# Performance work log

Hardware: AMD Instinct MI355X
Metric: run time of the kernel (lower is better)

Reference implementation:

```python
import jax, jax.numpy as jnp
import numpy as np

SELF_DIM = 36
ENT_DIM = 28
HID = 256


def setup_inputs() -> dict:
    key = jax.random.key(0)
    ks = jax.random.split(key, 12)
    B, agent_num, n_noisy = 32768, 20, 20
    obs_dim = SELF_DIM + ENT_DIM * (2 * agent_num - 1 + n_noisy)
    s = 0.02
    return {
        "x": jax.random.normal(ks[0], (B, obs_dim), dtype=jnp.float32),
        "Watt": jax.random.normal(ks[1], (ENT_DIM + SELF_DIM, 1), jnp.float32) * s,
        "batt": jnp.zeros((1,), jnp.float32),
        "We": jax.random.normal(ks[2], (ENT_DIM + SELF_DIM, HID), jnp.float32) * s,
        "be": jnp.zeros((HID,), jnp.float32),
        "Wse": jax.random.normal(ks[3], (2 * SELF_DIM, HID), jnp.float32) * s,
        "bse": jnp.zeros((HID,), jnp.float32),
        "Wg": jax.random.normal(ks[4], (3 * HID, 3), jnp.float32) * s,
        "bg": jnp.zeros((3,), jnp.float32),
        "Wo": jax.random.normal(ks[5], (2 * HID, HID), jnp.float32) * s,
        "bo": jnp.zeros((HID,), jnp.float32),
        "agent_num": agent_num,
    }


def reference(x, Watt, batt, We, be, Wse, bse, Wg, bg, Wo, bo, agent_num):
    B = x.shape[0]
    self_info = x[:, :SELF_DIM]  # [B,36]
    opp_end = SELF_DIM + ENT_DIM * agent_num
    par_end = opp_end + ENT_DIM * (agent_num - 1)
    opps = x[:, SELF_DIM:opp_end].reshape(B, agent_num, ENT_DIM)
    pars = x[:, opp_end:par_end].reshape(B, agent_num - 1, ENT_DIM)
    noisy = x[:, par_end:].reshape(B, -1, ENT_DIM)

    def pool(ent):
        # additive-attention pooling over one entity group
        n = ent.shape[1]
        os_ = jnp.concatenate(
            [jnp.broadcast_to(self_info[:, None, :], (B, n, SELF_DIM)), ent], axis=2
        )  # [B,n,64]
        att = jax.nn.softmax(os_ @ Watt + batt, axis=1)  # [B,n,1]
        es = os_ @ We + be  # [B,n,H]
        return jnp.sum(att * es, axis=1)  # [B,H]

    opp_e, par_e, noi_e = pool(opps), pool(pars), pool(noisy)
    group_e = jnp.stack([opp_e, par_e, noi_e], axis=1)  # [B,3,H]
    gw = jax.nn.softmax(
        jnp.concatenate([opp_e, par_e, noi_e], axis=1) @ Wg + bg, axis=1
    )  # [B,3]
    other = jnp.einsum("bg,bgh->bh", gw, group_e)  # [B,H]
    self_e = jnp.concatenate([self_info, self_info], axis=1) @ Wse + bse  # [B,H]
    obs_embedding = jnp.concatenate([other, self_e], axis=1)  # [B,2H]
    return obs_embedding @ Wo + bo
```

## Files before the change

kernel.cpp:

```cpp
#include <hip/hip_runtime.h>
#include <hip/hip_bf16.h>

#define SELF_D 36
#define ENT_D  28
#define HID    256
#define OBS    1688
#define NWAVES 8192

#define WS_A     0
#define WS_B     9216
#define WS_C     16384
#define WS_MSEL  16640
#define WS_MENT  16748
#define WS_CG    17000
#define WS_WATT  17008
#define WS_AT    17040
#define WS_BT    26256
#define WS_TOTAL 33424

__global__ __launch_bounds__(256)
void setup_kernel(const float* __restrict__ Watt, const float* __restrict__ We,
                  const float* __restrict__ be,  const float* __restrict__ Wse,
                  const float* __restrict__ bse, const float* __restrict__ Wg,
                  const float* __restrict__ bg,  const float* __restrict__ Wo,
                  const float* __restrict__ bo,  float* __restrict__ ws) {
  const int blk = blockIdx.x;
  const int c = threadIdx.x;
  if (blk < 36) {
    int k = blk;
    float acc = 0.f;
    for (int r = 0; r < 256; ++r) acc += We[k*256 + r] * Wo[r*256 + c];
    for (int r = 0; r < 256; ++r) acc += (Wse[k*256 + r] + Wse[(36+k)*256 + r]) * Wo[(256+r)*256 + c];
    ws[WS_A + k*256 + c] = acc;
    ws[WS_AT + c*36 + k] = acc;
  } else if (blk < 64) {
    int k = blk - 36;
    float acc = 0.f;
    for (int r = 0; r < 256; ++r) acc += We[(36+k)*256 + r] * Wo[r*256 + c];
    ws[WS_B + k*256 + c] = acc;
    ws[WS_BT + c*28 + k] = acc;
  } else if (blk == 64) {
    float acc = bo[c];
    for (int r = 0; r < 256; ++r) acc += be[r] * Wo[r*256 + c];
    for (int r = 0; r < 256; ++r) acc += bse[r] * Wo[(256+r)*256 + c];
    ws[WS_C + c] = acc;
  } else {
    for (int t = c; t < 391; t += 256) {
      if (t < 108) {
        int k = t / 3, j = t - 3*k;
        float acc = 0.f;
        for (int r = 0; r < 256; ++r) {
          float wg = Wg[r*3 + j] + Wg[(256+r)*3 + j] + Wg[(512+r)*3 + j];
          acc += We[k*256 + r] * wg;
        }
        ws[WS_MSEL + t] = acc;
      } else if (t < 360) {
        int idx = t - 108;
        int g = idx / 84, rem = idx - 84*g;
        int k = rem / 3, j = rem - 3*k;
        float acc = 0.f;
        for (int r = 0; r < 256; ++r) acc += We[(36+k)*256 + r] * Wg[(256*g + r)*3 + j];
        ws[WS_MENT + idx] = acc;
      } else if (t < 363) {
        int j = t - 360;
        float acc = bg[j];
        for (int r = 0; r < 256; ++r)
          acc += be[r] * (Wg[r*3 + j] + Wg[(256+r)*3 + j] + Wg[(512+r)*3 + j]);
        ws[WS_CG + j] = acc;
      } else {
        int k = t - 363;
        ws[WS_WATT + k] = Watt[36 + k];
      }
    }
  }
}

__global__ __launch_bounds__(256)
void pool_kernel(const float* __restrict__ x, const float* __restrict__ ws,
                 float* __restrict__ out, int B) {
  __shared__ float sM[360];
  __shared__ float satt[4][64];
  __shared__ float sebar[4][84];

  const int tid = threadIdx.x;
  const int w = tid >> 6, ln = tid & 63;

  for (int t = tid; t < 360; t += 256) sM[t] = ws[WS_MSEL + t];
  __syncthreads();

  const float* Wp = ws + WS_WATT;
  const float cg0 = ws[WS_CG + 0], cg1 = ws[WS_CG + 1], cg2 = ws[WS_CG + 2];

  const int ent_b = ln - (ln >= 40 ? 1 : 0);
  const bool valid_b = (ln < 60) && (ln != 39);

  for (int row = blockIdx.x * 4 + w; row < B; row += NWAVES) {
    const float* xr = x + (size_t)row * OBS;

    float l = -1e30f;
    {
      const float* e = xr + SELF_D + ENT_D * (valid_b ? ent_b : 0);
      float acc = 0.f;
#pragma unroll
      for (int q = 0; q < 7; ++q) {
        float4 v = ((const float4*)e)[q];
        acc += v.x*Wp[4*q] + v.y*Wp[4*q+1] + v.z*Wp[4*q+2] + v.w*Wp[4*q+3];
      }
      if (valid_b) l = acc;
    }
    float m = l;
#pragma unroll
    for (int off = 32; off; off >>= 1) m = fmaxf(m, __shfl_xor(m, off));
    satt[w][ln] = valid_b ? __expf(l - m) : 0.f;

#pragma unroll
    for (int pass = 0; pass < 2; ++pass) {
      int t = ln + pass * 64;
      if (t < 84) {
        int g = t / 28, k = t - 28 * g;
        int e0 = g * 20 - (g >> 1);
        const float* vb = xr + SELF_D + ENT_D * e0 + k;
        const float* pa = &satt[w][g * 20];
        float us = 0.f, uv = 0.f;
#pragma unroll
        for (int i = 0; i < 20; ++i) {
          float pp = pa[i];
          float vv = vb[ENT_D * i];
          us += pp; uv += pp * vv;
        }
        sebar[w][t] = uv / us;
      }
    }

    float gl = 0.f;
    {
      int j = ln >> 4, ch = ln & 15;
      if (j < 3 && ch < 15) {
#pragma unroll
        for (int q = 0; q < 8; ++q) {
          int c = q * 15 + ch;
          float v = (c < SELF_D) ? xr[c] : sebar[w][c - SELF_D];
          gl += v * sM[c * 3 + j];
        }
      }
#pragma unroll
      for (int off = 1; off < 16; off <<= 1) gl += __shfl_xor(gl, off);
    }
    float l0 = __shfl(gl, 0)  + cg0;
    float l1 = __shfl(gl, 16) + cg1;
    float l2 = __shfl(gl, 32) + cg2;
    float mm = fmaxf(l0, fmaxf(l1, l2));
    float e0x = __expf(l0 - mm), e1x = __expf(l1 - mm), e2x = __expf(l2 - mm);
    float inv = 1.f / (e0x + e1x + e2x);

    float fv;
    if (ln < SELF_D) {
      fv = xr[ln];
    } else {
      int k = ln - SELF_D;
      fv = (e0x * sebar[w][k] + e1x * sebar[w][28 + k] + e2x * sebar[w][56 + k]) * inv;
    }
    out[(size_t)row * HID + ln] = fv;
  }
}

#define PR_ROWS 32
#define PR_CH   8
__global__ __launch_bounds__(256)
void proj_kernel(const float* __restrict__ ws, float* __restrict__ out) {
  __shared__ __align__(16) float sf[PR_CH][64];
  const int tid = threadIdx.x;

  float4 Av[9], Bv[7];
#pragma unroll
  for (int q = 0; q < 9; ++q) Av[q] = ((const float4*)(ws + WS_AT + tid * 36))[q];
#pragma unroll
  for (int q = 0; q < 7; ++q) Bv[q] = ((const float4*)(ws + WS_BT + tid * 28))[q];
  const float cc = ws[WS_C + tid];

  const size_t row0 = (size_t)blockIdx.x * PR_ROWS;
  for (int chk = 0; chk < PR_ROWS / PR_CH; ++chk) {
    const size_t rbase = row0 + chk * PR_CH;
    if (tid < PR_CH * 16) {
      int r = tid >> 4, q = tid & 15;
      ((float4*)&sf[r][0])[q] = ((const float4*)(out + (rbase + r) * HID))[q];
    }
    __syncthreads();
#pragma unroll
    for (int r = 0; r < PR_CH; ++r) {
      float acc = cc;
      const float4* f4 = (const float4*)&sf[r][0];
#pragma unroll
      for (int q = 0; q < 9; ++q) {
        float4 s = f4[q];
        acc += Av[q].x*s.x + Av[q].y*s.y + Av[q].z*s.z + Av[q].w*s.w;
      }
#pragma unroll
      for (int q = 0; q < 7; ++q) {
        float4 s = f4[9 + q];
        acc += Bv[q].x*s.x + Bv[q].y*s.y + Bv[q].z*s.z + Bv[q].w*s.w;
      }
      out[(rbase + r) * HID + tid] = acc;
    }
    __syncthreads();
  }
}

extern "C" void kernel_launch(void* const* d_in, const int* in_sizes, int n_in,
                              void* d_out, int out_size, void* d_ws, size_t ws_size,
                              hipStream_t stream) {
  const float* x    = (const float*)d_in[0];
  const float* Watt = (const float*)d_in[1];
  const float* We   = (const float*)d_in[3];
  const float* be   = (const float*)d_in[4];
  const float* Wse  = (const float*)d_in[5];
  const float* bse  = (const float*)d_in[6];
  const float* Wg   = (const float*)d_in[7];
  const float* bg   = (const float*)d_in[8];
  const float* Wo   = (const float*)d_in[9];
  const float* bo   = (const float*)d_in[10];
  float* out = (float*)d_out;
  float* ws  = (float*)d_ws;
  const int B = in_sizes[0] / OBS;

  setup_kernel<<<66, 256, 0, stream>>>(Watt, We, be, Wse, bse, Wg, bg, Wo, bo, ws);
  pool_kernel<<<NWAVES / 4, 256, 0, stream>>>(x, ws, out, B);
  proj_kernel<<<B / PR_ROWS, 256, 0, stream>>>(ws, out);
}
```

Before: 104.1 us.

## Stage each input row into LDS with direct global-to-LDS loads in pool kernel

Measured after the change: 110.9 us. 1.07x slower.

```diff
diff --git a/kernel.cpp b/kernel.cpp
--- a/kernel.cpp
+++ b/kernel.cpp
@@ -78,40 +78,62 @@
 __global__ __launch_bounds__(256)
 void pool_kernel(const float* __restrict__ x, const float* __restrict__ ws,
                  float* __restrict__ out, int B) {
-  __shared__ float sM[360];
-  __shared__ float satt[4][64];
-  __shared__ float sebar[4][84];
+  __shared__ __align__(16) float tile[4][OBS];
+  __shared__ __align__(16) float satt[4][64];
+  __shared__ __align__(16) float sebar[4][84];
+  __shared__ __align__(16) float sW[28];
+  __shared__ __align__(16) float sM[360];
 
   const int tid = threadIdx.x;
   const int w = tid >> 6, ln = tid & 63;
 
   for (int t = tid; t < 360; t += 256) sM[t] = ws[WS_MSEL + t];
+  if (tid < 28) sW[tid] = ws[WS_WATT + tid];
   __syncthreads();
 
-  const float* Wp = ws + WS_WATT;
   const float cg0 = ws[WS_CG + 0], cg1 = ws[WS_CG + 1], cg2 = ws[WS_CG + 2];
 
-  const int ent_b = ln - (ln >= 40 ? 1 : 0);
-  const bool valid_b = (ln < 60) && (ln != 39);
+  const int ent_b  = ln - (ln >= 40 ? 1 : 0);
+  const bool valid = (ln < 60) && (ln != 39);
+  const int ent_r  = valid ? ent_b : 0;
+  int e7 = ent_r;
+  while (e7 >= 7) e7 -= 7;
+  const int gj = ln >> 4, gch = ln & 15;
+  const bool gact = (gj < 3) && (gch < 15);
 
   for (int row = blockIdx.x * 4 + w; row < B; row += NWAVES) {
     const float* xr = x + (size_t)row * OBS;
 
+#pragma unroll
+    for (int i = 0; i < 7; ++i) {
+      int idx = i * 64 + ln;
+      if (idx < OBS / 4) {
+        __builtin_amdgcn_global_load_lds(
+            (const __attribute__((address_space(1))) void*)(xr + idx * 4),
+            (__attribute__((address_space(3))) void*)(&tile[w][0] + idx * 4),
+            16, 0, 0);
+      }
+    }
+    asm volatile("s_waitcnt vmcnt(0)" ::: "memory");
+    __builtin_amdgcn_sched_barrier(0);
+
     float l = -1e30f;
     {
-      const float* e = xr + SELF_D + ENT_D * (valid_b ? ent_b : 0);
+      const float4* ep = (const float4*)&tile[w][SELF_D + ENT_D * ent_r];
+      const float4* w4 = (const float4*)sW;
       float acc = 0.f;
 #pragma unroll
-      for (int q = 0; q < 7; ++q) {
-        float4 v = ((const float4*)e)[q];
-        acc += v.x*Wp[4*q] + v.y*Wp[4*q+1] + v.z*Wp[4*q+2] + v.w*Wp[4*q+3];
-      }
-      if (valid_b) l = acc;
+      for (int t = 0; t < 7; ++t) {
+        int c = e7 + t; if (c >= 7) c -= 7;
+        float4 v = ep[c], wv = w4[c];
+        acc += v.x*wv.x + v.y*wv.y + v.z*wv.z + v.w*wv.w;
+      }
+      if (valid) l = acc;
     }
     float m = l;
 #pragma unroll
     for (int off = 32; off; off >>= 1) m = fmaxf(m, __shfl_xor(m, off));
-    satt[w][ln] = valid_b ? __expf(l - m) : 0.f;
+    satt[w][ln] = valid ? __expf(l - m) : 0.f;
 
 #pragma unroll
     for (int pass = 0; pass < 2; ++pass) {
@@ -119,7 +141,7 @@
       if (t < 84) {
         int g = t / 28, k = t - 28 * g;
         int e0 = g * 20 - (g >> 1);
-        const float* vb = xr + SELF_D + ENT_D * e0 + k;
+        const float* vb = &tile[w][SELF_D + ENT_D * e0 + k];
         const float* pa = &satt[w][g * 20];
         float us = 0.f, uv = 0.f;
 #pragma unroll
@@ -133,19 +155,16 @@
     }
 
     float gl = 0.f;
-    {
-      int j = ln >> 4, ch = ln & 15;
-      if (j < 3 && ch < 15) {
-#pragma unroll
-        for (int q = 0; q < 8; ++q) {
-          int c = q * 15 + ch;
-          float v = (c < SELF_D) ? xr[c] : sebar[w][c - SELF_D];
-          gl += v * sM[c * 3 + j];
-        }
-      }
-#pragma unroll
-      for (int off = 1; off < 16; off <<= 1) gl += __shfl_xor(gl, off);
-    }
+    if (gact) {
+#pragma unroll
+      for (int q = 0; q < 8; ++q) {
+        int c = q * 15 + gch;
+        float v = (c < SELF_D) ? tile[w][c] : sebar[w][c - SELF_D];
+        gl += v * sM[c * 3 + gj];
+      }
+    }
+#pragma unroll
+    for (int off = 1; off < 16; off <<= 1) gl += __shfl_xor(gl, off);
     float l0 = __shfl(gl, 0)  + cg0;
     float l1 = __shfl(gl, 16) + cg1;
     float l2 = __shfl(gl, 32) + cg2;
@@ -155,7 +174,7 @@
 
     float fv;
     if (ln < SELF_D) {
-      fv = xr[ln];
+      fv = tile[w][ln];
     } else {
       int k = ln - SELF_D;
       fv = (e0x * sebar[w][k] + e1x * sebar[w][28 + k] + e2x * sebar[w][56 + k]) * inv;
```

## Stage pool rows in transposed LDS tile with register prefetch of next row

Applied to the files above, without the earlier changes.

After: 106.9 us. +2.7%, slower.

```diff
diff --git a/kernel.cpp b/kernel.cpp
--- a/kernel.cpp
+++ b/kernel.cpp
@@ -6,6 +6,7 @@
 #define HID    256
 #define OBS    1688
 #define NWAVES 8192
+#define ETS    61
 
 #define WS_A     0
 #define WS_B     9216
@@ -78,74 +79,120 @@
 __global__ __launch_bounds__(256)
 void pool_kernel(const float* __restrict__ x, const float* __restrict__ ws,
                  float* __restrict__ out, int B) {
-  __shared__ float sM[360];
-  __shared__ float satt[4][64];
-  __shared__ float sebar[4][84];
+  __shared__ __align__(16) float ET[4][28*ETS + 4];
+  __shared__ __align__(16) float sself[4][40];
+  __shared__ __align__(16) float satt[4][64];
+  __shared__ __align__(16) float sebar[4][88];
+  __shared__ __align__(16) float sM[360];
 
   const int tid = threadIdx.x;
   const int w = tid >> 6, ln = tid & 63;
 
   for (int t = tid; t < 360; t += 256) sM[t] = ws[WS_MSEL + t];
+  if (ln < 28) ET[w][ln*ETS + 39] = 0.f;
   __syncthreads();
 
   const float* Wp = ws + WS_WATT;
   const float cg0 = ws[WS_CG + 0], cg1 = ws[WS_CG + 1], cg2 = ws[WS_CG + 2];
 
-  const int ent_b = ln - (ln >= 40 ? 1 : 0);
-  const bool valid_b = (ln < 60) && (ln != 39);
-
-  for (int row = blockIdx.x * 4 + w; row < B; row += NWAVES) {
-    const float* xr = x + (size_t)row * OBS;
+  int  eoff[7];
+  bool went[7];
+#pragma unroll
+  for (int i = 0; i < 7; ++i) {
+    int q = i*64 + ln;
+    went[i] = (q >= 9) && (q < 422);
+    int e = (q - 9) / 7, t = (q - 9) % 7;
+    int s = e + (e >= 39 ? 1 : 0);
+    eoff[i] = t*4*ETS + s;
+  }
+  const bool wself0 = (ln < 9);
+
+  const bool lval = (ln < 60) && (ln != 39);
+  const int  lcol = lval ? ln : 0;
+
+  const int  mg0 = ln / 28, mk0 = ln - 28*mg0;
+  const int  base0 = mk0*ETS + mg0*20;
+  const bool mv1 = (ln < 20);
+  const int  base1 = (ln + 8)*ETS + 40;
+
+  const int  gj = ln >> 4, gch = ln & 15;
+  const bool gact = (gj < 3) && (gch < 15);
+
+  const int row0 = blockIdx.x * 4 + w;
+
+  float4 pf[7];
+  if (row0 < B) {
+    const float4* xr = (const float4*)(x + (size_t)row0 * OBS);
+#pragma unroll
+    for (int i = 0; i < 7; ++i) { int idx = i*64 + ln; if (idx < 422) pf[i] = xr[idx]; }
+  }
+
+  for (int row = row0; row < B; row += NWAVES) {
+    if (wself0) *(float4*)&sself[w][ln*4] = pf[0];
+#pragma unroll
+    for (int i = 0; i < 7; ++i) {
+      if (went[i]) {
+        float* p = &ET[w][eoff[i]];
+        p[0]     = pf[i].x;
+        p[ETS]   = pf[i].y;
+        p[2*ETS] = pf[i].z;
+        p[3*ETS] = pf[i].w;
+      }
+    }
+
+    {
+      int nr = row + NWAVES;
+      if (nr < B) {
+        const float4* xn = (const float4*)(x + (size_t)nr * OBS);
+#pragma unroll
+        for (int i = 0; i < 7; ++i) { int idx = i*64 + ln; if (idx < 422) pf[i] = xn[idx]; }
+      }
+    }
+    asm volatile("" ::: "memory");
 
     float l = -1e30f;
     {
-      const float* e = xr + SELF_D + ENT_D * (valid_b ? ent_b : 0);
+      const float* cb = &ET[w][lcol];
       float acc = 0.f;
 #pragma unroll
-      for (int q = 0; q < 7; ++q) {
-        float4 v = ((const float4*)e)[q];
-        acc += v.x*Wp[4*q] + v.y*Wp[4*q+1] + v.z*Wp[4*q+2] + v.w*Wp[4*q+3];
-      }
-      if (valid_b) l = acc;
+      for (int k = 0; k < 28; ++k) acc += cb[k*ETS] * Wp[k];
+      if (lval) l = acc;
     }
     float m = l;
 #pragma unroll
     for (int off = 32; off; off >>= 1) m = fmaxf(m, __shfl_xor(m, off));
-    satt[w][ln] = valid_b ? __expf(l - m) : 0.f;
-
-#pragma unroll
-    for (int pass = 0; pass < 2; ++pass) {
-      int t = ln + pass * 64;
-      if (t < 84) {
-        int g = t / 28, k = t - 28 * g;
-        int e0 = g * 20 - (g >> 1);
-        const float* vb = xr + SELF_D + ENT_D * e0 + k;
-        const float* pa = &satt[w][g * 20];
-        float us = 0.f, uv = 0.f;
-#pragma unroll
-        for (int i = 0; i < 20; ++i) {
-          float pp = pa[i];
-          float vv = vb[ENT_D * i];
-          us += pp; uv += pp * vv;
-        }
-        sebar[w][t] = uv / us;
-      }
-    }
+    satt[w][ln] = lval ? __expf(l - m) : 0.f;
+    asm volatile("" ::: "memory");
+
+    {
+      const float* vb = &ET[w][base0];
+      const float* pa = &satt[w][mg0 * 20];
+      float us = 0.f, uv = 0.f;
+#pragma unroll
+      for (int i = 0; i < 20; ++i) { float pp = pa[i]; us += pp; uv += pp * vb[i]; }
+      sebar[w][ln] = uv / us;
+    }
+    if (mv1) {
+      const float* vb = &ET[w][base1];
+      const float* pa = &satt[w][40];
+      float us = 0.f, uv = 0.f;
+#pragma unroll
+      for (int i = 0; i < 20; ++i) { float pp = pa[i]; us += pp; uv += pp * vb[i]; }
+      sebar[w][ln + 64] = uv / us;
+    }
+    asm volatile("" ::: "memory");
 
     float gl = 0.f;
-    {
-      int j = ln >> 4, ch = ln & 15;
-      if (j < 3 && ch < 15) {
-#pragma unroll
-        for (int q = 0; q < 8; ++q) {
-          int c = q * 15 + ch;
-          float v = (c < SELF_D) ? xr[c] : sebar[w][c - SELF_D];
-          gl += v * sM[c * 3 + j];
-        }
-      }
-#pragma unroll
-      for (int off = 1; off < 16; off <<= 1) gl += __shfl_xor(gl, off);
-    }
+    if (gact) {
+#pragma unroll
+      for (int q = 0; q < 8; ++q) {
+        int c = q*15 + gch;
+        float v = (c < SELF_D) ? sself[w][c] : sebar[w][c - SELF_D];
+        gl += v * sM[c*3 + gj];
+      }
+    }
+#pragma unroll
+    for (int off = 1; off < 16; off <<= 1) gl += __shfl_xor(gl, off);
     float l0 = __shfl(gl, 0)  + cg0;
     float l1 = __shfl(gl, 16) + cg1;
     float l2 = __shfl(gl, 32) + cg2;
@@ -155,7 +202,7 @@
 
     float fv;
     if (ln < SELF_D) {
-      fv = xr[ln];
+      fv = sself[w][ln];
     } else {
       int k = ln - SELF_D;
       fv = (e0x * sebar[w][k] + e1x * sebar[w][28 + k] + e2x * sebar[w][56 + k]) * inv;
```
